# Performance work log

Hardware: AMD Instinct MI355X
Metric: run time of the kernel (lower is better)

## Reference

```python
import jax, jax.numpy as jnp
import numpy as np

N, E, G, D, L = 20000, 320000, 256, 256, 5
EPS = 1e-5


def _bn(h, g, b):
    # BatchNorm1d in training mode: biased batch statistics over the row dim
    m = h.mean(axis=0)
    v = jnp.mean((h - m) ** 2, axis=0)
    return g * (h - m) / jnp.sqrt(v + EPS) + b


def setup_inputs() -> dict:
    key = jax.random.key(0)
    ks = iter(jax.random.split(key, 40))

    def rn(shape, s=0.1):
        return jax.random.normal(next(ks), shape, dtype=jnp.float32) * s

    inp = {}
    inp['x_feats'] = jax.random.randint(next(ks), (N, 6), 0, 4)
    inp['edge_index'] = jax.random.randint(next(ks), (2, E), 0, N)
    inp['edge_attr'] = jax.random.randint(next(ks), (E, 5), 0, 2)
    inp['batch'] = jnp.sort(jax.random.randint(next(ks), (N,), 0, G))
    inp['nt1'] = rn((119, D)); inp['nt2'] = rn((4, D)); inp['nt3'] = rn((7, D))
    inp['nt4'] = rn((8, D)); inp['nt5'] = rn((5, D)); inp['nt6'] = rn((7, D))
    inp['et1'] = rn((L, 5, D)); inp['et2'] = rn((L, 4, D)); inp['et3'] = rn((L, 2, D))
    inp['et4'] = rn((L, 2, D)); inp['et5'] = rn((L, 2, D))
    inp['w1'] = rn((L, 2 * D, D)); inp['b1'] = rn((L, 2 * D))
    inp['w2'] = rn((L, D, 2 * D)); inp['b2'] = rn((L, D))
    inp['bng'] = 1.0 + rn((L, D)); inp['bnb'] = rn((L, D))
    inp['pw'] = rn((3, D, D)); inp['pg'] = 1.0 + rn((3, D)); inp['pb'] = rn((3, D))
    inp['ow1'] = rn((D // 2, D)); inp['ob1'] = rn((D // 2,))
    inp['ow2'] = rn((2, D // 2)); inp['ob2'] = rn((2,))
    return inp


def reference(x_feats, edge_index, edge_attr, batch,
              nt1, nt2, nt3, nt4, nt5, nt6,
              et1, et2, et3, et4, et5,
              w1, b1, w2, b2, bng, bnb,
              pw, pg, pb, ow1, ob1, ow2, ob2):
    n = x_feats.shape[0]
    # atom embedding: sum of 6 feature embeddings -> [N, D]
    h = (nt1[x_feats[:, 0]] + nt2[x_feats[:, 1]] + nt3[x_feats[:, 2]]
         + nt4[x_feats[:, 3]] + nt5[x_feats[:, 4]] + nt6[x_feats[:, 5]])
    src, dst = edge_index[0], edge_index[1]
    for l in range(L):
        # edge embedding for real edges: [E, D]
        e = (et1[l][edge_attr[:, 0]] + et2[l][edge_attr[:, 1]] + et3[l][edge_attr[:, 2]]
             + et4[l][edge_attr[:, 3]] + et5[l][edge_attr[:, 4]])
        # self-loop edges carry attr [4,0,0,0,0]
        self_e = et1[l][4] + et2[l][0] + et3[l][0] + et4[l][0] + et5[l][0]
        # message = x_j + e, scatter-add into destinations; self loops add h + self_e
        aggr = jax.ops.segment_sum(h[src] + e, dst, num_segments=n) + h + self_e
        # GIN MLP update: D -> 2D -> D
        hh = jax.nn.relu(aggr @ w1[l].T + b1[l]) @ w2[l].T + b2[l]
        # batchnorm then relu (dropout=0; the layer==num_layer branch is unreachable)
        h = jax.nn.relu(_bn(hh, bng[l], bnb[l]))
    # global mean pool over graphs
    counts = jax.ops.segment_sum(jnp.ones((n, 1), h.dtype), batch, num_segments=G)
    hg = jax.ops.segment_sum(h, batch, num_segments=G) / jnp.maximum(counts, 1.0)
    # proj head: (Linear no-bias, BN, ReLU) x2, then Linear no-bias + BN
    for i in range(3):
        hg = _bn(hg @ pw[i].T, pg[i], pb[i])
        if i < 2:
            hg = jax.nn.relu(hg)
    # output MLP: Linear -> Softplus -> Linear
    return jax.nn.softplus(hg @ ow1.T + ob1) @ ow2.T + ob2
```

## Files before the change

### kernel.cpp

```cpp
#include <hip/hip_runtime.h>

#define DD 256
#define TWO_D 512
#define NLAYER 5
#define NGRAPH 256
#define BNEPS 1e-5f

typedef __attribute__((ext_vector_type(8))) _Float16 half8;
typedef __attribute__((ext_vector_type(4))) _Float16 half4;
typedef __attribute__((ext_vector_type(4))) float f32x4;

__global__ __launch_bounds__(256) void prep_kernel(
    const int* __restrict__ xf,
    const float* __restrict__ nt1, const float* __restrict__ nt2,
    const float* __restrict__ nt3, const float* __restrict__ nt4,
    const float* __restrict__ nt5, const float* __restrict__ nt6,
    _Float16* __restrict__ h16,
    const float* __restrict__ w1, const float* __restrict__ w2,
    _Float16* __restrict__ w1h, _Float16* __restrict__ w2h,
    const float* __restrict__ et1, const float* __restrict__ et2,
    const float* __restrict__ et3, const float* __restrict__ et4,
    const float* __restrict__ et5, _Float16* __restrict__ etab,
    int* __restrict__ deg, int* __restrict__ zr, int zr_words,
    const int* __restrict__ ei, const int* __restrict__ ea,
    int* __restrict__ packed,
    int N, int E)
{
  const int t = threadIdx.x;
  const int b = blockIdx.x;
  const int B_EMB = N;
  const int B_WC  = 128;
  const int B_ET  = NLAYER * 33;
  const int B_ZR  = 96;

  if (b < B_EMB) {
    int i = b, j = t;
    int x0 = xf[i*6+0], x1 = xf[i*6+1], x2 = xf[i*6+2];
    int x3 = xf[i*6+3], x4 = xf[i*6+4], x5 = xf[i*6+5];
    float v = nt1[x0*DD+j] + nt2[x1*DD+j] + nt3[x2*DD+j]
            + nt4[x3*DD+j] + nt5[x4*DD+j] + nt6[x5*DD+j];
    h16[(size_t)i*DD + j] = (_Float16)v;
  } else if (b < B_EMB + B_WC) {
    int bid = b - B_EMB;
    int n = NLAYER * TWO_D * DD;
    for (int i = bid*256 + t; i < n; i += B_WC*256) {
      w1h[i] = (_Float16)w1[i];
      w2h[i] = (_Float16)w2[i];
    }
  } else if (b < B_EMB + B_WC + B_ET) {
    int bid = b - B_EMB - B_WC;
    int l = bid / 33, c = bid % 33;
    int j = t;
    int a0 = (c==32)?4:(c&1);
    int a1 = (c==32)?0:((c>>1)&1);
    int a2 = (c==32)?0:((c>>2)&1);
    int a3 = (c==32)?0:((c>>3)&1);
    int a4 = (c==32)?0:((c>>4)&1);
    etab[((size_t)l*33 + c)*DD + j] = (_Float16)(
        et1[(l*5+a0)*DD+j] + et2[(l*4+a1)*DD+j] + et3[(l*2+a2)*DD+j]
      + et4[(l*2+a3)*DD+j] + et5[(l*2+a4)*DD+j]);
  } else if (b < B_EMB + B_WC + B_ET + B_ZR) {
    int bid = b - B_EMB - B_WC - B_ET;
    int tw = N + zr_words;
    for (int i = bid*256 + t; i < tw; i += B_ZR*256) {
      if (i < N) deg[i] = 0;
      else zr[i - N] = 0;
    }
  } else {
    int bid = b - B_EMB - B_WC - B_ET - B_ZR;
    int e = bid*256 + t;
    if (e < E) {
      int src = ei[e];
      int code = (ea[e*5+0]&1) | ((ea[e*5+1]&1)<<1) | ((ea[e*5+2]&1)<<2)
               | ((ea[e*5+3]&1)<<3) | ((ea[e*5+4]&1)<<4);
      packed[e] = src | (code << 16);
    }
  }
}

__global__ __launch_bounds__(256) void hist_kernel(
    const int* __restrict__ ei, int* __restrict__ deg, int E)
{
  int e = blockIdx.x*256 + threadIdx.x;
  if (e < E) atomicAdd(&deg[ei[E + e]], 1);
}

__global__ __launch_bounds__(1024) void scan_kernel(
    const int* __restrict__ deg, int* __restrict__ row_start,
    int* __restrict__ cursor, int N)
{
  __shared__ int sh[1024];
  int t = threadIdx.x;
  const int CH = (N + 1023) >> 10;
  int base = t * CH;
  int lim = N - base; if (lim < 0) lim = 0; if (lim > CH) lim = CH;
  int s = 0;
  for (int i = 0; i < lim; ++i) s += deg[base + i];
  sh[t] = s;
  __syncthreads();
  for (int off = 1; off < 1024; off <<= 1) {
    int x = (t >= off) ? sh[t - off] : 0;
    __syncthreads();
    sh[t] += x;
    __syncthreads();
  }
  int run = t ? sh[t-1] : 0;
  for (int i = 0; i < lim; ++i) {
    row_start[base+i] = run; cursor[base+i] = run;
    run += deg[base+i];
  }
  if (t == 1023) row_start[N] = sh[1023];
}

__global__ __launch_bounds__(256) void scatter_kernel(
    const int* __restrict__ ei, const int* __restrict__ packed,
    int* __restrict__ cursor, int* __restrict__ esort, int E)
{
  int e = blockIdx.x*256 + threadIdx.x;
  if (e >= E) return;
  int dst = ei[E + e];
  int pos = atomicAdd(&cursor[dst], 1);
  esort[pos] = packed[e];
}

template<int APPLY_BN>
__global__ __launch_bounds__(256) void aggr_kernel(
    const _Float16* __restrict__ hsrc, const _Float16* __restrict__ etab_l,
    const int* __restrict__ row_start, const int* __restrict__ esort,
    const float* __restrict__ stats_prev, const float* __restrict__ g,
    const float* __restrict__ bb, float inv_n,
    _Float16* __restrict__ aggrh, int N)
{
  __shared__ __attribute__((aligned(16))) _Float16 se[33*DD];
  for (int i = threadIdx.x; i < 33*DD/8; i += 256)
    ((int4*)se)[i] = ((const int4*)etab_l)[i];
  __syncthreads();
  const int wave = threadIdx.x >> 6, lane = threadIdx.x & 63;
  const int c4 = lane << 2;
  float sc0=1.f, sc1=1.f, sc2=1.f, sc3=1.f, sh0=0.f, sh1=0.f, sh2=0.f, sh3=0.f;
  if (APPLY_BN) {
#define MKSC(k, SC, SH) { float m_ = stats_prev[c4+k]*inv_n;                      \
    float v_ = fmaxf(stats_prev[DD+c4+k]*inv_n - m_*m_, 0.f);                     \
    SC = g[c4+k]*rsqrtf(v_+BNEPS); SH = bb[c4+k] - m_*SC; }
    MKSC(0, sc0, sh0) MKSC(1, sc1, sh1) MKSC(2, sc2, sh2) MKSC(3, sc3, sh3)
#undef MKSC
  }
  const int W0 = blockIdx.x*4 + wave, NW = gridDim.x*4;

#define BNX(h4, o0, o1, o2, o3)                                           \
  { float t0_ = (float)(h4).x, t1_ = (float)(h4).y,                       \
          t2_ = (float)(h4).z, t3_ = (float)(h4).w;                       \
    if (APPLY_BN) {                                                       \
      t0_ = fmaxf(t0_*sc0 + sh0, 0.f); t1_ = fmaxf(t1_*sc1 + sh1, 0.f);  \
      t2_ = fmaxf(t2_*sc2 + sh2, 0.f); t3_ = fmaxf(t3_*sc3 + sh3, 0.f);  \
    }                                                                     \
    o0 = t0_; o1 = t1_; o2 = t2_; o3 = t3_; }

  for (int node = W0; node < N; node += NW) {
    int p  = row_start[node];
    int pe = row_start[node+1];
    const half4 hv = *(const half4*)(hsrc + (size_t)node*DD + c4);
    const half4 sv = *(const half4*)(se + 32*DD + c4);
    float ax, ay, az, aw;
    BNX(hv, ax, ay, az, aw);
    ax += (float)sv.x; ay += (float)sv.y; az += (float)sv.z; aw += (float)sv.w;
    for (; p + 4 <= pe; p += 4) {
      int pk0 = esort[p], pk1 = esort[p+1], pk2 = esort[p+2], pk3 = esort[p+3];
      const half4 h0 = *(const half4*)(hsrc + (size_t)(pk0 & 0xffff)*DD + c4);
      const half4 h1 = *(const half4*)(hsrc + (size_t)(pk1 & 0xffff)*DD + c4);
      const half4 h2 = *(const half4*)(hsrc + (size_t)(pk2 & 0xffff)*DD + c4);
      const half4 h3 = *(const half4*)(hsrc + (size_t)(pk3 & 0xffff)*DD + c4);
      const half4 e0 = *(const half4*)(se + (pk0 >> 16)*DD + c4);
      const half4 e1 = *(const half4*)(se + (pk1 >> 16)*DD + c4);
      const half4 e2 = *(const half4*)(se + (pk2 >> 16)*DD + c4);
      const half4 e3 = *(const half4*)(se + (pk3 >> 16)*DD + c4);
      float b0x,b0y,b0z,b0w, b1x,b1y,b1z,b1w, b2x,b2y,b2z,b2w, b3x,b3y,b3z,b3w;
      BNX(h0, b0x,b0y,b0z,b0w); BNX(h1, b1x,b1y,b1z,b1w);
      BNX(h2, b2x,b2y,b2z,b2w); BNX(h3, b3x,b3y,b3z,b3w);
      ax += (b0x+(float)e0.x) + (b1x+(float)e1.x) + (b2x+(float)e2.x) + (b3x+(float)e3.x);
      ay += (b0y+(float)e0.y) + (b1y+(float)e1.y) + (b2y+(float)e2.y) + (b3y+(float)e3.y);
      az += (b0z+(float)e0.z) + (b1z+(float)e1.z) + (b2z+(float)e2.z) + (b3z+(float)e3.z);
      aw += (b0w+(float)e0.w) + (b1w+(float)e1.w) + (b2w+(float)e2.w) + (b3w+(float)e3.w);
    }
    for (; p < pe; ++p) {
      int pk = esort[p];
      const half4 hx = *(const half4*)(hsrc + (size_t)(pk & 0xffff)*DD + c4);
      const half4 ex = *(const half4*)(se + (pk >> 16)*DD + c4);
      float bx, by, bz, bw;
      BNX(hx, bx, by, bz, bw);
      ax += bx + (float)ex.x; ay += by + (float)ex.y;
      az += bz + (float)ex.z; aw += bw + (float)ex.w;
    }
    half4 o;
    o.x = (_Float16)ax; o.y = (_Float16)ay; o.z = (_Float16)az; o.w = (_Float16)aw;
    *(half4*)(aggrh + (size_t)node*DD + c4) = o;
  }
#undef BNX
}

__global__ __launch_bounds__(256) void mlp_kernel(
    const _Float16* __restrict__ A,
    const _Float16* __restrict__ W1,
    const float* __restrict__ b1,
    const _Float16* __restrict__ W2,
    const float* __restrict__ b2,
    _Float16* __restrict__ O,
    float* __restrict__ stats,
    int Nreal)
{
  constexpr int PA = 264;
  constexpr int PH = 136;
  __shared__ __attribute__((aligned(16))) _Float16 sA[64*PA];
  __shared__ __attribute__((aligned(16))) _Float16 sH[64*PH];
  const int m0 = blockIdx.x << 6;
  const int t = threadIdx.x;
  const int w = t >> 6, lane = t & 63;
  const int r15 = lane & 15, quad = lane >> 4;

#pragma unroll
  for (int i = 0; i < 8; ++i) {
    int seg = (i << 8) + t;
    int row = seg >> 5, s = seg & 31;
    half8 v = *(const half8*)(A + (size_t)(m0 + row)*DD + (s << 3));
    *(half8*)(sA + row*PA + (s << 3)) = v;
  }
  __syncthreads();

  f32x4 acc2[4][4] = {};

#pragma unroll 1
  for (int c = 0; c < 4; ++c) {
    f32x4 acc1[4][2] = {};
#pragma unroll 2
    for (int ks = 0; ks < 8; ++ks) {
      half8 af[4], bf[2];
#pragma unroll
      for (int fm = 0; fm < 4; ++fm)
        af[fm] = *(const half8*)(sA + ((fm<<4) + r15)*PA + (ks<<5) + (quad<<3));
#pragma unroll
      for (int fn = 0; fn < 2; ++fn) {
        int wr = (c<<7) + (w<<5) + (fn<<4) + r15;
        bf[fn] = *(const half8*)(W1 + (size_t)wr*DD + (ks<<5) + (quad<<3));
      }
#pragma unroll
      for (int fm = 0; fm < 4; ++fm)
#pragma unroll
        for (int fn = 0; fn < 2; ++fn)
          acc1[fm][fn] = __builtin_amdgcn_mfma_f32_16x16x32_f16(af[fm], bf[fn], acc1[fm][fn], 0, 0, 0);
    }
#pragma unroll
    for (int fn = 0; fn < 2; ++fn) {
      int colL = (w<<5) + (fn<<4) + r15;
      float bv = b1[(c<<7) + colL];
#pragma unroll
      for (int fm = 0; fm < 4; ++fm) {
        int rb = (fm<<4) + (quad<<2);
#pragma unroll
        for (int r = 0; r < 4; ++r) {
          float v = fmaxf(acc1[fm][fn][r] + bv, 0.f);
          sH[(rb + r)*PH + colL] = (_Float16)v;
        }
      }
    }
    __syncthreads();
#pragma unroll 2
    for (int ks = 0; ks < 4; ++ks) {
      half8 af[4], bf[4];
#pragma unroll
      for (int fm = 0; fm < 4; ++fm)
        af[fm] = *(const half8*)(sH + ((fm<<4) + r15)*PH + (ks<<5) + (quad<<3));
#pragma unroll
      for (int fn = 0; fn < 4; ++fn) {
        int wr = (w<<6) + (fn<<4) + r15;
        bf[fn] = *(const half8*)(W2 + (size_t)wr*TWO_D + (c<<7) + (ks<<5) + (quad<<3));
      }
#pragma unroll
      for (int fm = 0; fm < 4; ++fm)
#pragma unroll
        for (int fn = 0; fn < 4; ++fn)
          acc2[fm][fn] = __builtin_amdgcn_mfma_f32_16x16x32_f16(af[fm], bf[fn], acc2[fm][fn], 0, 0, 0);
    }
    __syncthreads();
  }

#pragma unroll
  for (int fn = 0; fn < 4; ++fn) {
    int col = (w<<6) + (fn<<4) + r15;
    float bv = b2[col];
    float s1 = 0.f, s2 = 0.f;
#pragma unroll
    for (int fm = 0; fm < 4; ++fm) {
      int rb = (fm<<4) + (quad<<2);
#pragma unroll
      for (int r = 0; r < 4; ++r) {
        float v = acc2[fm][fn][r] + bv;
        sA[(rb + r)*PA + col] = (_Float16)v;
        if (m0 + rb + r < Nreal) { s1 += v; s2 += v*v; }
      }
    }
    s1 += __shfl_xor(s1, 16); s1 += __shfl_xor(s1, 32);
    s2 += __shfl_xor(s2, 16); s2 += __shfl_xor(s2, 32);
    if (lane < 16) { atomicAdd(&stats[col], s1); atomicAdd(&stats[DD + col], s2); }
  }
  __syncthreads();
#pragma unroll
  for (int i = 0; i < 8; ++i) {
    int seg = (i << 8) + t;
    int row = seg >> 5, s = seg & 31;
    half8 v = *(const half8*)(sA + row*PA + (s << 3));
    *(half8*)(O + (size_t)(m0 + row)*DD + (s << 3)) = v;
  }
}

__global__ __launch_bounds__(256) void pool_kernel(
    const _Float16* __restrict__ hh16, const float* __restrict__ stats_prev,
    const float* __restrict__ g, const float* __restrict__ bb, float inv_n,
    const int* __restrict__ batch,
    float* __restrict__ hgsum, int* __restrict__ hgcnt, int N)
{
  int j = threadIdx.x;
  float m = stats_prev[j]*inv_n;
  float var = fmaxf(stats_prev[DD+j]*inv_n - m*m, 0.f);
  float sc = g[j]*rsqrtf(var + BNEPS);
  float sh = bb[j] - m*sc;
  int r0 = blockIdx.x * 64;
  int cur = -1; float acc = 0.f; int run = 0;
  for (int r = 0; r < 64; ++r) {
    int row = r0 + r;
    if (row >= N) break;
    int gg = batch[row];
    if (gg != cur) {
      if (cur >= 0) {
        atomicAdd(&hgsum[(size_t)cur*DD + j], acc);
        if (j == 0) atomicAdd(&hgcnt[cur], run);
      }
      cur = gg; acc = 0.f; run = 0;
    }
    float v = (float)hh16[(size_t)row*DD + j];
    acc += fmaxf(v*sc + sh, 0.f);
    run++;
  }
  if (cur >= 0) {
    atomicAdd(&hgsum[(size_t)cur*DD + j], acc);
    if (j == 0) atomicAdd(&hgcnt[cur], run);
  }
}

template<int MODE>
__global__ __launch_bounds__(256) void proj_gemm_kernel(
    const float* __restrict__ in, const int* __restrict__ cnt,
    const float* __restrict__ pstat_prev,
    const float* __restrict__ gprev, const float* __restrict__ bprev,
    const float* __restrict__ W,
    float* __restrict__ outb, float* __restrict__ pstat)
{
  __shared__ float sA[16][17];
  __shared__ float sB[16][17];
  int tx = threadIdx.x, ty = threadIdx.y;
  int r = blockIdx.y*16 + ty;
  int c = blockIdx.x*16 + tx;
  float acc = 0.f;
  for (int k0 = 0; k0 < DD; k0 += 16) {
    int k = k0 + tx;
    float a = in[(size_t)r*DD + k];
    if (MODE == 0) {
      a /= (float)max(cnt[r], 1);
    } else {
      float m = pstat_prev[k] * (1.0f/NGRAPH);
      float var = fmaxf(pstat_prev[DD + k] * (1.0f/NGRAPH) - m*m, 0.f);
      float sc = gprev[k] * rsqrtf(var + BNEPS);
      a = fmaxf((a - m)*sc + bprev[k], 0.f);
    }
    sA[ty][tx] = a;
    sB[ty][tx] = W[(size_t)(blockIdx.x*16 + ty)*DD + k0 + tx];
    __syncthreads();
#pragma unroll
    for (int kk = 0; kk < 16; ++kk) acc += sA[ty][kk] * sB[tx][kk];
    __syncthreads();
  }
  outb[(size_t)r*DD + c] = acc;
  sA[ty][tx] = acc; sB[ty][tx] = acc*acc;
  __syncthreads();
  for (int o = 8; o > 0; o >>= 1) {
    if (ty < o) { sA[ty][tx] += sA[ty+o][tx]; sB[ty][tx] += sB[ty+o][tx]; }
    __syncthreads();
  }
  if (ty == 0) { atomicAdd(&pstat[c], sA[0][tx]); atomicAdd(&pstat[DD + c], sB[0][tx]); }
}

__global__ __launch_bounds__(128) void out_kernel(
    const float* __restrict__ t2, const float* __restrict__ pstat2,
    const float* __restrict__ g2, const float* __restrict__ b2p,
    const float* __restrict__ ow1, const float* __restrict__ ob1,
    const float* __restrict__ ow2, const float* __restrict__ ob2,
    float* __restrict__ outp)
{
  __shared__ float rowv[DD];
  __shared__ float z[128];
  int r = blockIdx.x, t = threadIdx.x;
#pragma unroll
  for (int half = 0; half < 2; ++half) {
    int j = t + half*128;
    float m = pstat2[j] * (1.0f/NGRAPH);
    float var = fmaxf(pstat2[DD + j] * (1.0f/NGRAPH) - m*m, 0.f);
    float sc = g2[j] * rsqrtf(var + BNEPS);
    rowv[j] = (t2[(size_t)r*DD + j] - m)*sc + b2p[j];
  }
  __syncthreads();
  float a = ob1[t];
  for (int k = 0; k < DD; ++k) a += rowv[k] * ow1[(size_t)t*DD + k];
  z[t] = fmaxf(a, 0.f) + log1pf(expf(-fabsf(a)));
  __syncthreads();
  if (t < 2) {
    float o = ob2[t];
    for (int k = 0; k < 128; ++k) o += z[k] * ow2[t*128 + k];
    outp[r*2 + t] = o;
  }
}

extern "C" void kernel_launch(void* const* d_in, const int* in_sizes, int n_in,
                              void* d_out, int out_size, void* d_ws, size_t ws_size,
                              hipStream_t stream)
{
  const int* x_feats = (const int*)d_in[0];
  const int* ei      = (const int*)d_in[1];
  const int* ea      = (const int*)d_in[2];
  const int* batch   = (const int*)d_in[3];
  const float* nt1 = (const float*)d_in[4];
  const float* nt2 = (const float*)d_in[5];
  const float* nt3 = (const float*)d_in[6];
  const float* nt4 = (const float*)d_in[7];
  const float* nt5 = (const float*)d_in[8];
  const float* nt6 = (const float*)d_in[9];
  const float* et1 = (const float*)d_in[10];
  const float* et2 = (const float*)d_in[11];
  const float* et3 = (const float*)d_in[12];
  const float* et4 = (const float*)d_in[13];
  const float* et5 = (const float*)d_in[14];
  const float* w1  = (const float*)d_in[15];
  const float* b1  = (const float*)d_in[16];
  const float* w2  = (const float*)d_in[17];
  const float* b2  = (const float*)d_in[18];
  const float* bng = (const float*)d_in[19];
  const float* bnb = (const float*)d_in[20];
  const float* pw  = (const float*)d_in[21];
  const float* pg  = (const float*)d_in[22];
  const float* pb  = (const float*)d_in[23];
  const float* ow1 = (const float*)d_in[24];
  const float* ob1 = (const float*)d_in[25];
  const float* ow2 = (const float*)d_in[26];
  const float* ob2 = (const float*)d_in[27];

  const int N = in_sizes[0] / 6;
  const int E = in_sizes[1] / 2;
  const int Mp = ((N + 63) >> 6) << 6;

  unsigned char* wp = (unsigned char*)d_ws;
  size_t off = 0;
  auto carve = [&](size_t bytes) -> void* {
    void* p = wp + off;
    off += (bytes + 255) & ~(size_t)255;
    return p;
  };

  _Float16* h16      = (_Float16*)carve((size_t)N * DD * 2);
  _Float16* aggrh    = (_Float16*)carve((size_t)Mp * DD * 2);
  _Float16* hh16     = (_Float16*)carve((size_t)Mp * DD * 2);
  _Float16* w1h      = (_Float16*)carve((size_t)NLAYER * TWO_D * DD * 2);
  _Float16* w2h      = (_Float16*)carve((size_t)NLAYER * TWO_D * DD * 2);
  _Float16* etabg    = (_Float16*)carve((size_t)NLAYER * 33 * DD * 2);
  int* deg           = (int*)carve((size_t)N * 4);
  int* row_start     = (int*)carve((size_t)(N + 1) * 4);
  int* cursor        = (int*)carve((size_t)N * 4);
  int* packed        = (int*)carve((size_t)E * 4);
  int* esort         = (int*)carve((size_t)E * 4);
  float* stats       = (float*)carve((size_t)NLAYER * 2 * DD * 4);
  float* hgsum       = (float*)carve((size_t)NGRAPH * DD * 4);
  int* hgcnt         = (int*)carve((size_t)NGRAPH * 4);
  float* pstats      = (float*)carve(3 * 2 * DD * 4);
  const int ZR_WORDS = NLAYER*2*DD + NGRAPH*DD + NGRAPH + 3*2*DD;
  float* hgA         = (float*)carve((size_t)NGRAPH * DD * 4);
  float* hgB         = (float*)carve((size_t)NGRAPH * DD * 4);
  float* t0c         = (float*)carve((size_t)NGRAPH * DD * 4);
  (void)ws_size; (void)n_in; (void)out_size;

  const int EB = (E + 255) / 256;
  const float inv_n = 1.0f / (float)N;

  const int PREP_BLOCKS = N + 128 + NLAYER*33 + 96 + EB;
  prep_kernel<<<PREP_BLOCKS, 256, 0, stream>>>(
      x_feats, nt1, nt2, nt3, nt4, nt5, nt6, h16,
      w1, w2, w1h, w2h,
      et1, et2, et3, et4, et5, etabg,
      deg, (int*)stats, ZR_WORDS,
      ei, ea, packed, N, E);
  hist_kernel<<<EB, 256, 0, stream>>>(ei, deg, E);
  scan_kernel<<<1, 1024, 0, stream>>>(deg, row_start, cursor, N);
  scatter_kernel<<<EB, 256, 0, stream>>>(ei, packed, cursor, esort, E);

  const int MB = Mp >> 6;
  for (int l = 0; l < NLAYER; ++l) {
    float* st_prev = stats + (size_t)(l-1)*2*DD;
    float* st_cur  = stats + (size_t)l*2*DD;
    if (l == 0) {
      aggr_kernel<0><<<2048, 256, 0, stream>>>(h16, etabg, row_start, esort,
                                               nullptr, nullptr, nullptr, inv_n,
                                               aggrh, N);
    } else {
      aggr_kernel<1><<<2048, 256, 0, stream>>>(hh16, etabg + (size_t)l*33*DD,
                                               row_start, esort,
                                               st_prev, bng + (l-1)*DD, bnb + (l-1)*DD,
                                               inv_n, aggrh, N);
    }
    mlp_kernel<<<MB, 256, 0, stream>>>(
        aggrh, w1h + (size_t)l*TWO_D*DD, b1 + l*TWO_D,
        w2h + (size_t)l*DD*TWO_D, b2 + l*DD,
        hh16, st_cur, N);
  }

  pool_kernel<<<(N + 63) / 64, 256, 0, stream>>>(
      hh16, stats + (size_t)(NLAYER-1)*2*DD, bng + (NLAYER-1)*DD, bnb + (NLAYER-1)*DD,
      inv_n, batch, hgsum, hgcnt, N);

  dim3 pgrid(16, 16), pblk(16, 16);
  proj_gemm_kernel<0><<<pgrid, pblk, 0, stream>>>(
      hgsum, hgcnt, nullptr, nullptr, nullptr,
      pw + 0*DD*DD, hgA, pstats + 0*2*DD);
  proj_gemm_kernel<1><<<pgrid, pblk, 0, stream>>>(
      hgA, nullptr, pstats + 0*2*DD, pg + 0*DD, pb + 0*DD,
      pw + 1*DD*DD, hgB, pstats + 1*2*DD);
  proj_gemm_kernel<1><<<pgrid, pblk, 0, stream>>>(
      hgB, nullptr, pstats + 1*2*DD, pg + 1*DD, pb + 1*DD,
      pw + 2*DD*DD, t0c, pstats + 2*2*DD);
  out_kernel<<<NGRAPH, 128, 0, stream>>>(
      t0c, pstats + 2*2*DD, pg + 2*DD, pb + 2*DD,
      ow1, ob1, ow2, ob2, (float*)d_out);
}
```

Measured before the change: 583.0 us.

## Pre-swizzle MLP weights into MFMA fragment order and shrink row tile to 32

Weights are now written by the prep kernel in a fragment-major layout, so each lane loads its MFMA B operand with one contiguous 16-byte read. The MLP kernel drops from 64-row tiles with 4 waves to 32-row tiles with 8 waves, giving twice as many blocks for better occupancy. LDS padding is replaced by an XOR swizzle to avoid bank conflicts. The trade-off is more weight traffic per output row, since each block now reloads the full weights for only 32 rows, and fewer MFMAs per wave to hide latency.

```diff
diff --git a/kernel.cpp b/kernel.cpp
--- a/kernel.cpp
+++ b/kernel.cpp
@@ -9,6 +9,8 @@
 typedef __attribute__((ext_vector_type(8))) _Float16 half8;
 typedef __attribute__((ext_vector_type(4))) _Float16 half4;
 typedef __attribute__((ext_vector_type(4))) float f32x4;
+
+#define MFMA16 __builtin_amdgcn_mfma_f32_16x16x32_f16
 
 __global__ __launch_bounds__(256) void prep_kernel(
     const int* __restrict__ xf,
@@ -17,7 +19,7 @@
     const float* __restrict__ nt5, const float* __restrict__ nt6,
     _Float16* __restrict__ h16,
     const float* __restrict__ w1, const float* __restrict__ w2,
-    _Float16* __restrict__ w1h, _Float16* __restrict__ w2h,
+    _Float16* __restrict__ w1f, _Float16* __restrict__ w2f,
     const float* __restrict__ et1, const float* __restrict__ et2,
     const float* __restrict__ et3, const float* __restrict__ et4,
     const float* __restrict__ et5, _Float16* __restrict__ etab,
@@ -44,8 +46,13 @@
     int bid = b - B_EMB;
     int n = NLAYER * TWO_D * DD;
     for (int i = bid*256 + t; i < n; i += B_WC*256) {
-      w1h[i] = (_Float16)w1[i];
-      w2h[i] = (_Float16)w2[i];
+      int l = i >> 17, rem = i & 131071;
+      int r = rem >> 8, k = rem & 255;
+      int o1 = (l<<17) + (((r>>4)<<3) + (k>>5))*512 + ((((k>>3)&3)<<4) + (r&15))*8 + (k&7);
+      w1f[o1] = (_Float16)w1[i];
+      int r2 = rem >> 9, k2 = rem & 511;
+      int o2 = (l<<17) + (((r2>>4)<<4) + (k2>>5))*512 + ((((k2>>3)&3)<<4) + (r2&15))*8 + (k2&7);
+      w2f[o2] = (_Float16)w2[i];
     }
   } else if (b < B_EMB + B_WC + B_ET) {
     int bid = b - B_EMB - B_WC;
@@ -198,116 +205,100 @@
 #undef BNX
 }
 
-__global__ __launch_bounds__(256) void mlp_kernel(
+__global__ __launch_bounds__(512) void mlp_kernel(
     const _Float16* __restrict__ A,
-    const _Float16* __restrict__ W1,
+    const _Float16* __restrict__ W1f,
     const float* __restrict__ b1,
-    const _Float16* __restrict__ W2,
+    const _Float16* __restrict__ W2f,
     const float* __restrict__ b2,
     _Float16* __restrict__ O,
     float* __restrict__ stats,
     int Nreal)
 {
-  constexpr int PA = 264;
-  constexpr int PH = 136;
-  __shared__ __attribute__((aligned(16))) _Float16 sA[64*PA];
-  __shared__ __attribute__((aligned(16))) _Float16 sH[64*PH];
-  const int m0 = blockIdx.x << 6;
+  __shared__ __attribute__((aligned(16))) _Float16 sA[32*256];
+  __shared__ __attribute__((aligned(16))) _Float16 sH[32*128];
+  const int m0 = blockIdx.x << 5;
   const int t = threadIdx.x;
   const int w = t >> 6, lane = t & 63;
   const int r15 = lane & 15, quad = lane >> 4;
-
-#pragma unroll
-  for (int i = 0; i < 8; ++i) {
-    int seg = (i << 8) + t;
+  const int rx = r15 & 7;
+
+#pragma unroll
+  for (int i = 0; i < 2; ++i) {
+    int seg = (i << 9) + t;
     int row = seg >> 5, s = seg & 31;
     half8 v = *(const half8*)(A + (size_t)(m0 + row)*DD + (s << 3));
-    *(half8*)(sA + row*PA + (s << 3)) = v;
-  }
-  __syncthreads();
-
-  f32x4 acc2[4][4] = {};
-
+    *(half8*)(sA + (row << 8) + ((s ^ (row & 7)) << 3)) = v;
+  }
+  __syncthreads();
+
+  f32x4 acc2[2][2] = {};
 #pragma unroll 1
   for (int c = 0; c < 4; ++c) {
-    f32x4 acc1[4][2] = {};
-#pragma unroll 2
+    f32x4 acc1[2] = {};
+    const _Float16* W1b = W1f + (((c << 3) + w) << 12);
+#pragma unroll
     for (int ks = 0; ks < 8; ++ks) {
-      half8 af[4], bf[2];
-#pragma unroll
-      for (int fm = 0; fm < 4; ++fm)
-        af[fm] = *(const half8*)(sA + ((fm<<4) + r15)*PA + (ks<<5) + (quad<<3));
-#pragma unroll
-      for (int fn = 0; fn < 2; ++fn) {
-        int wr = (c<<7) + (w<<5) + (fn<<4) + r15;
-        bf[fn] = *(const half8*)(W1 + (size_t)wr*DD + (ks<<5) + (quad<<3));
-      }
-#pragma unroll
-      for (int fm = 0; fm < 4; ++fm)
-#pragma unroll
-        for (int fn = 0; fn < 2; ++fn)
-          acc1[fm][fn] = __builtin_amdgcn_mfma_f32_16x16x32_f16(af[fm], bf[fn], acc1[fm][fn], 0, 0, 0);
-    }
-#pragma unroll
-    for (int fn = 0; fn < 2; ++fn) {
-      int colL = (w<<5) + (fn<<4) + r15;
-      float bv = b1[(c<<7) + colL];
-#pragma unroll
-      for (int fm = 0; fm < 4; ++fm) {
-        int rb = (fm<<4) + (quad<<2);
+      int so = (((ks << 2) + quad) ^ rx) << 3;
+      half8 a0 = *(const half8*)(sA + (r15 << 8) + so);
+      half8 a1 = *(const half8*)(sA + ((16 + r15) << 8) + so);
+      half8 bf = *(const half8*)(W1b + (ks << 9) + (lane << 3));
+      acc1[0] = MFMA16(a0, bf, acc1[0], 0, 0, 0);
+      acc1[1] = MFMA16(a1, bf, acc1[1], 0, 0, 0);
+    }
+    {
+      int colL = (w << 4) + r15;
+      float bv = b1[(c << 7) + colL];
+#pragma unroll
+      for (int fm = 0; fm < 2; ++fm)
 #pragma unroll
         for (int r = 0; r < 4; ++r) {
-          float v = fmaxf(acc1[fm][fn][r] + bv, 0.f);
-          sH[(rb + r)*PH + colL] = (_Float16)v;
+          int row = (fm << 4) + (quad << 2) + r;
+          float v = fmaxf(acc1[fm][r] + bv, 0.f);
+          sH[(row << 7) + ((((colL >> 3) ^ (row & 7)) << 3)) + (colL & 7)] = (_Float16)v;
         }
-      }
-    }
-    __syncthreads();
-#pragma unroll 2
+    }
+    __syncthreads();
+#pragma unroll
     for (int ks = 0; ks < 4; ++ks) {
-      half8 af[4], bf[4];
-#pragma unroll
-      for (int fm = 0; fm < 4; ++fm)
-        af[fm] = *(const half8*)(sH + ((fm<<4) + r15)*PH + (ks<<5) + (quad<<3));
-#pragma unroll
-      for (int fn = 0; fn < 4; ++fn) {
-        int wr = (w<<6) + (fn<<4) + r15;
-        bf[fn] = *(const half8*)(W2 + (size_t)wr*TWO_D + (c<<7) + (ks<<5) + (quad<<3));
-      }
-#pragma unroll
-      for (int fm = 0; fm < 4; ++fm)
-#pragma unroll
-        for (int fn = 0; fn < 4; ++fn)
-          acc2[fm][fn] = __builtin_amdgcn_mfma_f32_16x16x32_f16(af[fm], bf[fn], acc2[fm][fn], 0, 0, 0);
-    }
-    __syncthreads();
-  }
-
-#pragma unroll
-  for (int fn = 0; fn < 4; ++fn) {
-    int col = (w<<6) + (fn<<4) + r15;
+      int so = (((ks << 2) + quad) ^ rx) << 3;
+      half8 a0 = *(const half8*)(sH + (r15 << 7) + so);
+      half8 a1 = *(const half8*)(sH + ((16 + r15) << 7) + so);
+      int ks2 = (c << 2) + ks;
+      half8 b0 = *(const half8*)(W2f + ((((w << 1) + 0) << 13)) + (ks2 << 9) + (lane << 3));
+      half8 b1v = *(const half8*)(W2f + ((((w << 1) + 1) << 13)) + (ks2 << 9) + (lane << 3));
+      acc2[0][0] = MFMA16(a0, b0, acc2[0][0], 0, 0, 0);
+      acc2[0][1] = MFMA16(a0, b1v, acc2[0][1], 0, 0, 0);
+      acc2[1][0] = MFMA16(a1, b0, acc2[1][0], 0, 0, 0);
+      acc2[1][1] = MFMA16(a1, b1v, acc2[1][1], 0, 0, 0);
+    }
+    __syncthreads();
+  }
+
+#pragma unroll
+  for (int fn = 0; fn < 2; ++fn) {
+    int col = (w << 5) + (fn << 4) + r15;
     float bv = b2[col];
     float s1 = 0.f, s2 = 0.f;
 #pragma unroll
-    for (int fm = 0; fm < 4; ++fm) {
-      int rb = (fm<<4) + (quad<<2);
+    for (int fm = 0; fm < 2; ++fm)
 #pragma unroll
       for (int r = 0; r < 4; ++r) {
+        int row = (fm << 4) + (quad << 2) + r;
         float v = acc2[fm][fn][r] + bv;
-        sA[(rb + r)*PA + col] = (_Float16)v;
-        if (m0 + rb + r < Nreal) { s1 += v; s2 += v*v; }
+        sA[(row << 8) + (((col >> 3) ^ (row & 7)) << 3) + (col & 7)] = (_Float16)v;
+        if (m0 + row < Nreal) { s1 += v; s2 += v*v; }
       }
-    }
     s1 += __shfl_xor(s1, 16); s1 += __shfl_xor(s1, 32);
     s2 += __shfl_xor(s2, 16); s2 += __shfl_xor(s2, 32);
     if (lane < 16) { atomicAdd(&stats[col], s1); atomicAdd(&stats[DD + col], s2); }
   }
   __syncthreads();
 #pragma unroll
-  for (int i = 0; i < 8; ++i) {
-    int seg = (i << 8) + t;
+  for (int i = 0; i < 2; ++i) {
+    int seg = (i << 9) + t;
     int row = seg >> 5, s = seg & 31;
-    half8 v = *(const half8*)(sA + row*PA + (s << 3));
+    half8 v = *(const half8*)(sA + (row << 8) + ((s ^ (row & 7)) << 3));
     *(half8*)(O + (size_t)(m0 + row)*DD + (s << 3)) = v;
   }
 }
@@ -453,7 +444,7 @@
 
   const int N = in_sizes[0] / 6;
   const int E = in_sizes[1] / 2;
-  const int Mp = ((N + 63) >> 6) << 6;
+  const int Mp = ((N + 31) >> 5) << 5;
 
   unsigned char* wp = (unsigned char*)d_ws;
   size_t off = 0;
@@ -466,8 +457,8 @@
   _Float16* h16      = (_Float16*)carve((size_t)N * DD * 2);
   _Float16* aggrh    = (_Float16*)carve((size_t)Mp * DD * 2);
   _Float16* hh16     = (_Float16*)carve((size_t)Mp * DD * 2);
-  _Float16* w1h      = (_Float16*)carve((size_t)NLAYER * TWO_D * DD * 2);
-  _Float16* w2h      = (_Float16*)carve((size_t)NLAYER * TWO_D * DD * 2);
+  _Float16* w1f      = (_Float16*)carve((size_t)NLAYER * TWO_D * DD * 2);
+  _Float16* w2f      = (_Float16*)carve((size_t)NLAYER * TWO_D * DD * 2);
   _Float16* etabg    = (_Float16*)carve((size_t)NLAYER * 33 * DD * 2);
   int* deg           = (int*)carve((size_t)N * 4);
   int* row_start     = (int*)carve((size_t)(N + 1) * 4);
@@ -490,7 +481,7 @@
   const int PREP_BLOCKS = N + 128 + NLAYER*33 + 96 + EB;
   prep_kernel<<<PREP_BLOCKS, 256, 0, stream>>>(
       x_feats, nt1, nt2, nt3, nt4, nt5, nt6, h16,
-      w1, w2, w1h, w2h,
+      w1, w2, w1f, w2f,
       et1, et2, et3, et4, et5, etabg,
       deg, (int*)stats, ZR_WORDS,
       ei, ea, packed, N, E);
@@ -498,7 +489,7 @@
   scan_kernel<<<1, 1024, 0, stream>>>(deg, row_start, cursor, N);
   scatter_kernel<<<EB, 256, 0, stream>>>(ei, packed, cursor, esort, E);
 
-  const int MB = Mp >> 6;
+  const int MB = Mp >> 5;
   for (int l = 0; l < NLAYER; ++l) {
     float* st_prev = stats + (size_t)(l-1)*2*DD;
     float* st_cur  = stats + (size_t)l*2*DD;
@@ -512,9 +503,9 @@
                                                st_prev, bng + (l-1)*DD, bnb + (l-1)*DD,
                                                inv_n, aggrh, N);
     }
-    mlp_kernel<<<MB, 256, 0, stream>>>(
-        aggrh, w1h + (size_t)l*TWO_D*DD, b1 + l*TWO_D,
-        w2h + (size_t)l*DD*TWO_D, b2 + l*DD,
+    mlp_kernel<<<MB, 512, 0, stream>>>(
+        aggrh, w1f + ((size_t)l << 17), b1 + l*TWO_D,
+        w2f + ((size_t)l << 17), b2 + l*DD,
         hh16, st_cur, N);
   }
 
```

Result: faster. 558.7 us (-4.2%).
